# Performance work log

Hardware: AMD Instinct MI355X
Metric: run time of the kernel (lower is better)

Reference implementation:

```python
import jax, jax.numpy as jnp
import numpy as np

NUM_HEADS = 12
HEAD_DIM = 128
DIM = NUM_HEADS * HEAD_DIM  # 1536
ROTARY_DIM = HEAD_DIM       # partial_rotary_factor = 1
BASE = 10000.0
EPS = 1e-6


def rms_norm(x, scale):
    # RMSNorm over the full inner dim (applied before head split), Flux-style QKNorm
    var = jnp.mean(x * x, axis=-1, keepdims=True)
    return x * jax.lax.rsqrt(var + EPS) * scale


def rope_cos_sin(n):
    half = ROTARY_DIM // 2
    inv_freq = 1.0 / (BASE ** (jnp.arange(0, half, dtype=jnp.float32) / half))
    ang = jnp.arange(n, dtype=jnp.float32)[:, None] * inv_freq[None, :]  # [n, half]
    # broadcast over [b, n, h, half]
    return jnp.cos(ang)[None, :, None, :], jnp.sin(ang)[None, :, None, :]


def apply_rope(x, cos, sin):
    # x: [b, n, h, d]; rotate first ROTARY_DIM dims (NeoX half-split)
    half = ROTARY_DIM // 2
    x1 = x[..., :half]
    x2 = x[..., half:ROTARY_DIM]
    rest = x[..., ROTARY_DIM:]
    out = jnp.concatenate([x1 * cos - x2 * sin, x2 * cos + x1 * sin], axis=-1)
    if rest.shape[-1]:
        out = jnp.concatenate([out, rest], axis=-1)
    return out


def setup_inputs() -> dict:
    key = jax.random.key(0)
    ks = jax.random.split(key, 12)
    b, s_in, s_ctx = 2, 2048, 256
    sd = 0.02
    return {
        "input": jax.random.normal(ks[0], (b, s_in, DIM), dtype=jnp.float32),
        "context": jax.random.normal(ks[1], (b, s_ctx, DIM), dtype=jnp.float32),
        "W_qkv_in": jax.random.normal(ks[2], (DIM, 3 * DIM), dtype=jnp.float32) * sd,
        "b_qkv_in": jnp.zeros((3 * DIM,), dtype=jnp.float32),
        "W_qkv_ctx": jax.random.normal(ks[3], (DIM, 3 * DIM), dtype=jnp.float32) * sd,
        "b_qkv_ctx": jnp.zeros((3 * DIM,), dtype=jnp.float32),
        "qs_in": jnp.ones((DIM,), dtype=jnp.float32),
        "ks_in": jnp.ones((DIM,), dtype=jnp.float32),
        "qs_ctx": jnp.ones((DIM,), dtype=jnp.float32),
        "ks_ctx": jnp.ones((DIM,), dtype=jnp.float32),
        "W_out_in": jax.random.normal(ks[4], (DIM, DIM), dtype=jnp.float32) * sd,
        "b_out_in": jnp.zeros((DIM,), dtype=jnp.float32),
        "W_out_ctx": jax.random.normal(ks[5], (DIM, DIM), dtype=jnp.float32) * sd,
        "b_out_ctx": jnp.zeros((DIM,), dtype=jnp.float32),
    }


def reference(input, context, W_qkv_in, b_qkv_in, W_qkv_ctx, b_qkv_ctx,
              qs_in, ks_in, qs_ctx, ks_ctx,
              W_out_in, b_out_in, W_out_ctx, b_out_ctx):
    b = input.shape[0]
    s_ctx = context.shape[1]

    qi, ki, vi = jnp.split(input @ W_qkv_in + b_qkv_in, 3, axis=-1)
    qc, kc, vc = jnp.split(context @ W_qkv_ctx + b_qkv_ctx, 3, axis=-1)

    qi = rms_norm(qi, qs_in)
    ki = rms_norm(ki, ks_in)
    qc = rms_norm(qc, qs_ctx)
    kc = rms_norm(kc, ks_ctx)

    # concatenated joint sequence: context first, then input
    q = jnp.concatenate([qc, qi], axis=1)
    k = jnp.concatenate([kc, ki], axis=1)
    v = jnp.concatenate([vc, vi], axis=1)
    n = q.shape[1]

    q = q.reshape(b, n, NUM_HEADS, HEAD_DIM)
    k = k.reshape(b, n, NUM_HEADS, HEAD_DIM)
    v = v.reshape(b, n, NUM_HEADS, HEAD_DIM)

    cos, sin = rope_cos_sin(n)
    q = apply_rope(q, cos, sin)
    k = apply_rope(k, cos, sin)

    scale = HEAD_DIM ** -0.5
    attn = jnp.einsum("bqhd,bkhd->bhqk", q, k) * scale
    attn = jax.nn.softmax(attn, axis=-1)
    out = jnp.einsum("bhqk,bkhd->bqhd", attn, v).reshape(b, n, DIM)

    input_output = out[:, s_ctx:, :] @ W_out_in + b_out_in
    context_output = out[:, :s_ctx, :] @ W_out_ctx + b_out_ctx
    return (input_output, context_output)
```

## Files before the change

kernel.cpp:

```cpp
#include <hip/hip_runtime.h>
#include <hip/hip_bf16.h>

typedef __hip_bfloat16 bf16;
typedef __attribute__((ext_vector_type(8))) short short8;
typedef __attribute__((ext_vector_type(4))) float f32x4;

#define DIMC 1536
#define NQKV 4608
#define NH   12
#define HD   128
#define NTOK 2304
#define SCTX 256
#define SIN  2048
#define BATCH 2

__device__ __forceinline__ float bf2f(unsigned short u) {
    return __uint_as_float(((unsigned int)u) << 16);
}
__device__ __forceinline__ unsigned short f2bfu(float f) {
    bf16 h = (bf16)f; return *(unsigned short*)&h;
}

#define GLOAD16(gp, lp) __builtin_amdgcn_global_load_lds(                      \
    (__attribute__((address_space(1))) void*)(gp),                             \
    (__attribute__((address_space(3))) void*)(lp), 16, 0, 0)

__global__ __launch_bounds__(256) void cvt_bf16(
    const float* __restrict__ X, unsigned short* __restrict__ Y, int n4)
{
    int i = blockIdx.x * 256 + threadIdx.x;
    if (i < n4) {
        float4 v = ((const float4*)X)[i];
        union { unsigned short u[4]; uint2 p; } o;
        o.u[0] = f2bfu(v.x); o.u[1] = f2bfu(v.y);
        o.u[2] = f2bfu(v.z); o.u[3] = f2bfu(v.w);
        ((uint2*)Y)[i] = o.p;
    }
}

__global__ __launch_bounds__(256) void transpose_cvt(
    const float* __restrict__ W, unsigned short* __restrict__ Wt, int K, int N)
{
    __shared__ float tile[32][33];
    int n0 = blockIdx.x * 32, k0 = blockIdx.y * 32;
    int tx = threadIdx.x & 31, ty = threadIdx.x >> 5;
    #pragma unroll
    for (int i = 0; i < 4; ++i) {
        int kk = ty + i * 8;
        tile[kk][tx] = W[(size_t)(k0 + kk) * N + n0 + tx];
    }
    __syncthreads();
    #pragma unroll
    for (int i = 0; i < 4; ++i) {
        int nn = ty + i * 8;
        Wt[(size_t)(n0 + nn) * K + k0 + tx] = f2bfu(tile[tx][nn]);
    }
}

__device__ __forceinline__ void storeC(float* p, float v) { *p = v; }
__device__ __forceinline__ void storeC(unsigned short* p, float v) { *p = f2bfu(v); }

template <typename CT>
__global__ __launch_bounds__(256) void gemm_mfma(
    const unsigned short* __restrict__ A, const unsigned short* __restrict__ Wt,
    const float* __restrict__ bias, CT* __restrict__ C,
    int N, int K, int S, int aStr, int aOff, int cStr, int cOff)
{
    __shared__ __align__(16) unsigned short a_lds[128 * 32];
    __shared__ __align__(16) unsigned short b_lds[128 * 32];

    int tid = threadIdx.x;
    int wv = tid >> 6, lane = tid & 63;
    int wm = wv >> 1, wn = wv & 1;
    int quad = lane >> 4, l16 = lane & 15;
    int bm = blockIdx.y * 128, bn = blockIdx.x * 128;

    int m0 = tid >> 2;
    int c  = (tid & 3) ^ ((m0 >> 1) & 3);
    int r0 = bm + m0, r1 = bm + m0 + 64;
    size_t apA0 = ((size_t)((r0 / S) * aStr + aOff + (r0 % S))) * (size_t)K + c * 8;
    size_t apA1 = ((size_t)((r1 / S) * aStr + aOff + (r1 % S))) * (size_t)K + c * 8;
    size_t apB0 = (size_t)(bn + m0) * K + c * 8;
    size_t apB1 = (size_t)(bn + m0 + 64) * K + c * 8;

    unsigned short* ldsA0 = &a_lds[(wv * 64) * 8];
    unsigned short* ldsA1 = &a_lds[(256 + wv * 64) * 8];
    unsigned short* ldsB0 = &b_lds[(wv * 64) * 8];
    unsigned short* ldsB1 = &b_lds[(256 + wv * 64) * 8];

    int gA[4], gB[4];
    #pragma unroll
    for (int mt = 0; mt < 4; ++mt) {
        int m = wm * 64 + mt * 16 + l16;
        gA[mt] = (m * 4 + (quad ^ ((m >> 1) & 3))) * 8;
    }
    #pragma unroll
    for (int nt = 0; nt < 4; ++nt) {
        int n = wn * 64 + nt * 16 + l16;
        gB[nt] = (n * 4 + (quad ^ ((n >> 1) & 3))) * 8;
    }

    f32x4 acc[4][4];
    #pragma unroll
    for (int mt = 0; mt < 4; ++mt)
        #pragma unroll
        for (int nt = 0; nt < 4; ++nt) acc[mt][nt] = (f32x4){0.f, 0.f, 0.f, 0.f};

    for (int k0 = 0; k0 < K; k0 += 32) {
        GLOAD16(A + apA0 + k0, ldsA0);
        GLOAD16(A + apA1 + k0, ldsA1);
        GLOAD16(Wt + apB0 + k0, ldsB0);
        GLOAD16(Wt + apB1 + k0, ldsB1);
        __syncthreads();

        short8 af[4], bfr[4];
        #pragma unroll
        for (int mt = 0; mt < 4; ++mt) af[mt] = *(const short8*)&a_lds[gA[mt]];
        #pragma unroll
        for (int nt = 0; nt < 4; ++nt) bfr[nt] = *(const short8*)&b_lds[gB[nt]];
        #pragma unroll
        for (int mt = 0; mt < 4; ++mt)
            #pragma unroll
            for (int nt = 0; nt < 4; ++nt)
                acc[mt][nt] = __builtin_amdgcn_mfma_f32_16x16x32_bf16(
                    af[mt], bfr[nt], acc[mt][nt], 0, 0, 0);
        __syncthreads();
    }

    float bv[4];
    #pragma unroll
    for (int nt = 0; nt < 4; ++nt) bv[nt] = bias[bn + wn * 64 + nt * 16 + l16];
    #pragma unroll
    for (int mt = 0; mt < 4; ++mt) {
        #pragma unroll
        for (int r = 0; r < 4; ++r) {
            int row = bm + wm * 64 + mt * 16 + quad * 4 + r;
            size_t crow = (size_t)((row / S) * cStr + cOff + (row % S));
            CT* cp = C + crow * (size_t)N + bn + wn * 64 + l16;
            #pragma unroll
            for (int nt = 0; nt < 4; ++nt)
                storeC(cp + nt * 16, acc[mt][nt][r] + bv[nt]);
        }
    }
}

__global__ __launch_bounds__(256) void rms_rope_pack(
    const unsigned short* __restrict__ QKV,
    const float* __restrict__ qs_in, const float* __restrict__ ks_in,
    const float* __restrict__ qs_ctx, const float* __restrict__ ks_ctx,
    bf16* __restrict__ Q, bf16* __restrict__ K)
{
    __shared__ float qrow[DIMC];
    __shared__ float krow[DIMC];
    __shared__ float rq[4], rk[4];

    int token = blockIdx.x;
    int b = token / NTOK;
    int p = token % NTOK;
    bool is_ctx = (p < SCTX);
    const float* qs = is_ctx ? qs_ctx : qs_in;
    const float* ks = is_ctx ? ks_ctx : ks_in;

    int t = threadIdx.x;
    const unsigned short* row = QKV + (size_t)token * NQKV;

    float ssq_q = 0.f, ssq_k = 0.f;
    #pragma unroll
    for (int i = 0; i < 6; ++i) {
        int c = t + 256 * i;
        float q = bf2f(row[c]);
        float k = bf2f(row[DIMC + c]);
        qrow[c] = q; krow[c] = k;
        ssq_q += q * q; ssq_k += k * k;
    }
    for (int o = 32; o > 0; o >>= 1) {
        ssq_q += __shfl_down(ssq_q, o);
        ssq_k += __shfl_down(ssq_k, o);
    }
    if ((t & 63) == 0) { rq[t >> 6] = ssq_q; rk[t >> 6] = ssq_k; }
    __syncthreads();
    float sq = rq[0] + rq[1] + rq[2] + rq[3];
    float sk = rk[0] + rk[1] + rk[2] + rk[3];
    float invq = rsqrtf(sq * (1.0f / DIMC) + 1e-6f);
    float invk = rsqrtf(sk * (1.0f / DIMC) + 1e-6f);

    #pragma unroll
    for (int i = 0; i < 6; ++i) {
        int c = t + 256 * i;
        int h = c >> 7, d = c & 127;
        int j = d & 63;
        float inv_freq = powf(10000.0f, -(float)j * (1.0f / 64.0f));
        float ang = (float)p * inv_freq;
        float sn, cs;
        sincosf(ang, &sn, &cs);
        int pc = (d < 64) ? (c + 64) : (c - 64);

        float self_q = qrow[c]  * invq * qs[c];
        float part_q = qrow[pc] * invq * qs[pc];
        float qo = (d < 64) ? (self_q * cs - part_q * sn)
                            : (self_q * cs + part_q * sn);

        float self_k = krow[c]  * invk * ks[c];
        float part_k = krow[pc] * invk * ks[pc];
        float ko = (d < 64) ? (self_k * cs - part_k * sn)
                            : (self_k * cs + part_k * sn);

        size_t qi = ((size_t)(b * NH + h) * NTOK + p) * HD + d;
        Q[qi] = (bf16)qo;
        K[qi] = (bf16)ko;
    }
}

__global__ __launch_bounds__(256) void vt_pack(
    const unsigned short* __restrict__ QKV, unsigned short* __restrict__ Vt)
{
    __shared__ unsigned short tileT[128][72];

    int pt = blockIdx.x % (NTOK / 64);
    int bh = blockIdx.x / (NTOK / 64);
    int b = bh / NH, h = bh % NH;
    int p0 = pt * 64;

    int t = threadIdx.x, wv = t >> 6, l = t & 63;

    const unsigned short* src =
        QKV + (size_t)(b * NTOK + p0 + l) * NQKV + 2 * DIMC + h * HD;
    #pragma unroll
    for (int it = 0; it < 4; ++it) {
        int c = it * 4 + wv;
        short8 v = *(const short8*)(src + c * 8);
        const unsigned short* vp = (const unsigned short*)&v;
        #pragma unroll
        for (int i = 0; i < 8; ++i) tileT[c * 8 + i][l] = vp[i];
    }
    __syncthreads();

    int d = t >> 1, jh = (t & 1) * 32;
    unsigned short* dst = Vt + ((size_t)bh * HD + d) * NTOK + p0 + jh;
    #pragma unroll
    for (int k = 0; k < 4; ++k) {
        short8 v = *(const short8*)&tileT[d][jh + k * 8];
        *(short8*)(dst + k * 8) = v;
    }
}

__global__ __launch_bounds__(256, 2) void attn_mfma(
    const unsigned short* __restrict__ Qh,
    const unsigned short* __restrict__ Kh,
    const unsigned short* __restrict__ Vth,
    bf16* __restrict__ O)
{
    __shared__ __align__(16) unsigned short k_lds[64 * 128];
    __shared__ __align__(16) unsigned short v_lds[128 * 64];
    __shared__ __align__(16) unsigned short p_lds[4][32][72];
    __shared__ float bc[4][32];

    int tid = threadIdx.x;
    int wv = tid >> 6, lane = tid & 63;
    int quad = lane >> 4, l16 = lane & 15;

    int qt = blockIdx.x % (NTOK / 128);
    int bh = blockIdx.x / (NTOK / 128);
    int b = bh / NH, h = bh % NH;
    int p0 = qt * 128;
    int qw = p0 + wv * 32;

    const unsigned short* Kbh = Kh + (size_t)bh * NTOK * HD;
    const unsigned short* Vbh = Vth + (size_t)bh * HD * NTOK;

    short8 qf[2][4];
    #pragma unroll
    for (int mt = 0; mt < 2; ++mt) {
        const unsigned short* qrow =
            Qh + ((size_t)bh * NTOK + qw + mt * 16 + l16) * HD + quad * 8;
        #pragma unroll
        for (int dk = 0; dk < 4; ++dk) qf[mt][dk] = *(const short8*)(qrow + dk * 32);
    }

    float m_r[2][4], l_r[2][4];
    f32x4 oac[8][2];
    #pragma unroll
    for (int mt = 0; mt < 2; ++mt)
        #pragma unroll
        for (int r = 0; r < 4; ++r) { m_r[mt][r] = -1e30f; l_r[mt][r] = 0.f; }
    #pragma unroll
    for (int md = 0; md < 8; ++md)
        #pragma unroll
        for (int nt = 0; nt < 2; ++nt) oac[md][nt] = (f32x4){0.f, 0.f, 0.f, 0.f};

    const float cscale = 0.08838834764831845f * 1.44269504088896f;

    int jrowK = wv * 4 + (lane >> 4);
    int cK = (lane & 15) ^ jrowK;
    int dV = wv * 8 + (lane >> 3);
    int cV = (lane & 7) ^ (lane >> 3);

    for (int j0 = 0; j0 < NTOK; j0 += 64) {
        #pragma unroll
        for (int it = 0; it < 4; ++it)
            GLOAD16(Kbh + (size_t)(j0 + it * 16 + jrowK) * HD + cK * 8,
                    &k_lds[(it * 256 + wv * 64) * 8]);
        #pragma unroll
        for (int it = 0; it < 4; ++it)
            GLOAD16(Vbh + (size_t)(it * 32 + dV) * NTOK + j0 + cV * 8,
                    &v_lds[(it * 256 + wv * 64) * 8]);
        __syncthreads();

        f32x4 s[2][4];
        #pragma unroll
        for (int n = 0; n < 4; ++n) {
            int jl = n * 16 + l16;
            f32x4 a0 = (f32x4){0.f, 0.f, 0.f, 0.f};
            f32x4 a1 = (f32x4){0.f, 0.f, 0.f, 0.f};
            #pragma unroll
            for (int dk = 0; dk < 4; ++dk) {
                short8 kf = *(const short8*)&k_lds[(jl * 16 + ((dk * 4 + quad) ^ l16)) * 8];
                a0 = __builtin_amdgcn_mfma_f32_16x16x32_bf16(qf[0][dk], kf, a0, 0, 0, 0);
                a1 = __builtin_amdgcn_mfma_f32_16x16x32_bf16(qf[1][dk], kf, a1, 0, 0, 0);
            }
            s[0][n] = a0; s[1][n] = a1;
        }

        float alpha[2][4], rs[2][4];
        #pragma unroll
        for (int mt = 0; mt < 2; ++mt) {
            #pragma unroll
            for (int r = 0; r < 4; ++r) {
                float t = fmaxf(fmaxf(s[mt][0][r], s[mt][1][r]),
                                fmaxf(s[mt][2][r], s[mt][3][r]));
                t = fmaxf(t, __shfl_xor(t, 1));
                t = fmaxf(t, __shfl_xor(t, 2));
                t = fmaxf(t, __shfl_xor(t, 4));
                t = fmaxf(t, __shfl_xor(t, 8));
                float mn = fmaxf(m_r[mt][r], t * cscale);
                alpha[mt][r] = exp2f(m_r[mt][r] - mn);
                m_r[mt][r] = mn;
                rs[mt][r] = 0.f;
            }
        }

        #pragma unroll
        for (int mt = 0; mt < 2; ++mt)
            #pragma unroll
            for (int n = 0; n < 4; ++n) {
                #pragma unroll
                for (int r = 0; r < 4; ++r) {
                    float e = exp2f(s[mt][n][r] * cscale - m_r[mt][r]);
                    rs[mt][r] += e;
                    p_lds[wv][mt * 16 + quad * 4 + r][n * 16 + l16] = f2bfu(e);
                }
            }
        #pragma unroll
        for (int mt = 0; mt < 2; ++mt)
            #pragma unroll
            for (int r = 0; r < 4; ++r) {
                float t = rs[mt][r];
                t += __shfl_xor(t, 1);
                t += __shfl_xor(t, 2);
                t += __shfl_xor(t, 4);
                t += __shfl_xor(t, 8);
                l_r[mt][r] = l_r[mt][r] * alpha[mt][r] + t;
            }

        if (l16 == 0) {
            #pragma unroll
            for (int mt = 0; mt < 2; ++mt)
                #pragma unroll
                for (int r = 0; r < 4; ++r)
                    bc[wv][mt * 16 + quad * 4 + r] = alpha[mt][r];
        }
        float al[2];
        #pragma unroll
        for (int nt = 0; nt < 2; ++nt) al[nt] = bc[wv][nt * 16 + l16];
        #pragma unroll
        for (int md = 0; md < 8; ++md)
            #pragma unroll
            for (int nt = 0; nt < 2; ++nt) {
                oac[md][nt][0] *= al[nt]; oac[md][nt][1] *= al[nt];
                oac[md][nt][2] *= al[nt]; oac[md][nt][3] *= al[nt];
            }

        #pragma unroll
        for (int kt = 0; kt < 2; ++kt) {
            short8 pf[2];
            #pragma unroll
            for (int nt = 0; nt < 2; ++nt)
                pf[nt] = *(const short8*)&p_lds[wv][nt * 16 + l16][kt * 32 + quad * 8];
            #pragma unroll
            for (int md = 0; md < 8; ++md) {
                int dl = md * 16 + l16;
                short8 vf = *(const short8*)&v_lds[(dl * 8 + ((kt * 4 + quad) ^ (l16 & 7))) * 8];
                #pragma unroll
                for (int nt = 0; nt < 2; ++nt)
                    oac[md][nt] = __builtin_amdgcn_mfma_f32_16x16x32_bf16(
                        vf, pf[nt], oac[md][nt], 0, 0, 0);
            }
        }
        __syncthreads();
    }

    if (l16 == 0) {
        #pragma unroll
        for (int mt = 0; mt < 2; ++mt)
            #pragma unroll
            for (int r = 0; r < 4; ++r)
                bc[wv][mt * 16 + quad * 4 + r] = l_r[mt][r];
    }
    float il[2];
    #pragma unroll
    for (int nt = 0; nt < 2; ++nt) il[nt] = 1.0f / bc[wv][nt * 16 + l16];

    #pragma unroll
    for (int md = 0; md < 8; ++md)
        #pragma unroll
        for (int nt = 0; nt < 2; ++nt) {
            int q = qw + nt * 16 + l16;
            union { unsigned short u[4]; uint2 v; } pk;
            #pragma unroll
            for (int r = 0; r < 4; ++r) pk.u[r] = f2bfu(oac[md][nt][r] * il[nt]);
            *(uint2*)((unsigned short*)O +
                      ((size_t)(b * NTOK) + q) * DIMC + h * HD + md * 16 + quad * 4) = pk.v;
        }
}

extern "C" void kernel_launch(void* const* d_in, const int* in_sizes, int n_in,
                              void* d_out, int out_size, void* d_ws, size_t ws_size,
                              hipStream_t stream)
{
    const float* input     = (const float*)d_in[0];
    const float* context   = (const float*)d_in[1];
    const float* W_qkv_in  = (const float*)d_in[2];
    const float* b_qkv_in  = (const float*)d_in[3];
    const float* W_qkv_ctx = (const float*)d_in[4];
    const float* b_qkv_ctx = (const float*)d_in[5];
    const float* qs_in     = (const float*)d_in[6];
    const float* ks_in     = (const float*)d_in[7];
    const float* qs_ctx    = (const float*)d_in[8];
    const float* ks_ctx    = (const float*)d_in[9];
    const float* W_out_in  = (const float*)d_in[10];
    const float* b_out_in  = (const float*)d_in[11];
    const float* W_out_ctx = (const float*)d_in[12];
    const float* b_out_ctx = (const float*)d_in[13];
    float* out = (float*)d_out;

    char* ws = (char*)d_ws;
    unsigned short* QKVb = (unsigned short*)ws;
    bf16*           Ob   = (bf16*)ws;
    unsigned short* Qb   = (unsigned short*)(ws + 42467328);
    unsigned short* Kb   = Qb + (size_t)BATCH * NH * NTOK * HD;
    unsigned short* Vtb  = Kb + (size_t)BATCH * NH * NTOK * HD;
    unsigned short* AbIn  = (unsigned short*)(ws + 84934656);
    unsigned short* AbCtx = AbIn + (size_t)BATCH * SIN * DIMC;
    unsigned short* WtOutIn  = (unsigned short*)(ws + 84934656);
    unsigned short* WtOutCtx = WtOutIn + (size_t)DIMC * DIMC;
    unsigned short* WtQkvIn  = (unsigned short*)(ws + 99090432);
    unsigned short* WtQkvCtx = (unsigned short*)(ws + 113246208);

    cvt_bf16<<<(BATCH * SIN * DIMC / 4 + 255) / 256, 256, 0, stream>>>(
        input, AbIn, BATCH * SIN * DIMC / 4);
    cvt_bf16<<<(BATCH * SCTX * DIMC / 4 + 255) / 256, 256, 0, stream>>>(
        context, AbCtx, BATCH * SCTX * DIMC / 4);
    transpose_cvt<<<dim3(NQKV / 32, DIMC / 32), 256, 0, stream>>>(W_qkv_in, WtQkvIn, DIMC, NQKV);
    transpose_cvt<<<dim3(NQKV / 32, DIMC / 32), 256, 0, stream>>>(W_qkv_ctx, WtQkvCtx, DIMC, NQKV);

    gemm_mfma<unsigned short><<<dim3(NQKV / 128, (BATCH * SIN) / 128), 256, 0, stream>>>(
        AbIn, WtQkvIn, b_qkv_in, QKVb, NQKV, DIMC, SIN, SIN, 0, NTOK, SCTX);
    gemm_mfma<unsigned short><<<dim3(NQKV / 128, (BATCH * SCTX) / 128), 256, 0, stream>>>(
        AbCtx, WtQkvCtx, b_qkv_ctx, QKVb, NQKV, DIMC, SCTX, SCTX, 0, NTOK, 0);

    rms_rope_pack<<<BATCH * NTOK, 256, 0, stream>>>(
        QKVb, qs_in, ks_in, qs_ctx, ks_ctx, (bf16*)Qb, (bf16*)Kb);
    vt_pack<<<BATCH * NH * (NTOK / 64), 256, 0, stream>>>(QKVb, Vtb);

    attn_mfma<<<BATCH * NH * (NTOK / 128), 256, 0, stream>>>(Qb, Kb, Vtb, Ob);

    transpose_cvt<<<dim3(DIMC / 32, DIMC / 32), 256, 0, stream>>>(W_out_in, WtOutIn, DIMC, DIMC);
    transpose_cvt<<<dim3(DIMC / 32, DIMC / 32), 256, 0, stream>>>(W_out_ctx, WtOutCtx, DIMC, DIMC);

    gemm_mfma<float><<<dim3(DIMC / 128, (BATCH * SIN) / 128), 256, 0, stream>>>(
        (const unsigned short*)Ob, WtOutIn, b_out_in, out,
        DIMC, DIMC, SIN, NTOK, SCTX, SIN, 0);
    gemm_mfma<float><<<dim3(DIMC / 128, (BATCH * SCTX) / 128), 256, 0, stream>>>(
        (const unsigned short*)Ob, WtOutCtx, b_out_ctx, out + (size_t)BATCH * SIN * DIMC,
        DIMC, DIMC, SCTX, NTOK, 0, SCTX, 0);
}
```

Measured before the change: 555.9 us.

## Shrink attention query tile, merge conversion launches, precompute RoPE tables

Result: slower. 571.8 us (+2.9%).

```diff
diff --git a/kernel.cpp b/kernel.cpp
--- a/kernel.cpp
+++ b/kernel.cpp
@@ -25,23 +25,29 @@
     (__attribute__((address_space(1))) void*)(gp),                             \
     (__attribute__((address_space(3))) void*)(lp), 16, 0, 0)
 
-__global__ __launch_bounds__(256) void cvt_bf16(
-    const float* __restrict__ X, unsigned short* __restrict__ Y, int n4)
+__global__ __launch_bounds__(256) void cvt_both(
+    const float* __restrict__ X0, unsigned short* __restrict__ Y0, int n4_0,
+    const float* __restrict__ X1, unsigned short* __restrict__ Y1, int n4_1)
 {
     int i = blockIdx.x * 256 + threadIdx.x;
-    if (i < n4) {
-        float4 v = ((const float4*)X)[i];
-        union { unsigned short u[4]; uint2 p; } o;
-        o.u[0] = f2bfu(v.x); o.u[1] = f2bfu(v.y);
-        o.u[2] = f2bfu(v.z); o.u[3] = f2bfu(v.w);
-        ((uint2*)Y)[i] = o.p;
-    }
-}
-
-__global__ __launch_bounds__(256) void transpose_cvt(
-    const float* __restrict__ W, unsigned short* __restrict__ Wt, int K, int N)
+    const float* X; unsigned short* Y;
+    if (i < n4_0) { X = X0; Y = Y0; }
+    else { i -= n4_0; if (i >= n4_1) return; X = X1; Y = Y1; }
+    float4 v = ((const float4*)X)[i];
+    union { unsigned short u[4]; uint2 p; } o;
+    o.u[0] = f2bfu(v.x); o.u[1] = f2bfu(v.y);
+    o.u[2] = f2bfu(v.z); o.u[3] = f2bfu(v.w);
+    ((uint2*)Y)[i] = o.p;
+}
+
+__global__ __launch_bounds__(256) void transpose_cvt_pair(
+    const float* __restrict__ W0, unsigned short* __restrict__ Wt0,
+    const float* __restrict__ W1, unsigned short* __restrict__ Wt1,
+    int K, int N)
 {
     __shared__ float tile[32][33];
+    const float* W = blockIdx.z ? W1 : W0;
+    unsigned short* Wt = blockIdx.z ? Wt1 : Wt0;
     int n0 = blockIdx.x * 32, k0 = blockIdx.y * 32;
     int tx = threadIdx.x & 31, ty = threadIdx.x >> 5;
     #pragma unroll
@@ -55,6 +61,19 @@
         int nn = ty + i * 8;
         Wt[(size_t)(n0 + nn) * K + k0 + tx] = f2bfu(tile[tx][nn]);
     }
+}
+
+__global__ __launch_bounds__(256) void rope_table(
+    float* __restrict__ cost, float* __restrict__ sint)
+{
+    int idx = blockIdx.x * 256 + threadIdx.x;
+    if (idx >= NTOK * 64) return;
+    int p = idx >> 6, j = idx & 63;
+    float inv_freq = powf(10000.0f, -(float)j * (1.0f / 64.0f));
+    float ang = (float)p * inv_freq;
+    float sn, cs;
+    sincosf(ang, &sn, &cs);
+    cost[idx] = cs; sint[idx] = sn;
 }
 
 __device__ __forceinline__ void storeC(float* p, float v) { *p = v; }
@@ -148,6 +167,7 @@
     const unsigned short* __restrict__ QKV,
     const float* __restrict__ qs_in, const float* __restrict__ ks_in,
     const float* __restrict__ qs_ctx, const float* __restrict__ ks_ctx,
+    const float* __restrict__ cost, const float* __restrict__ sint,
     bf16* __restrict__ Q, bf16* __restrict__ K)
 {
     __shared__ float qrow[DIMC];
@@ -187,12 +207,10 @@
     #pragma unroll
     for (int i = 0; i < 6; ++i) {
         int c = t + 256 * i;
-        int h = c >> 7, d = c & 127;
+        int d = c & 127;
         int j = d & 63;
-        float inv_freq = powf(10000.0f, -(float)j * (1.0f / 64.0f));
-        float ang = (float)p * inv_freq;
-        float sn, cs;
-        sincosf(ang, &sn, &cs);
+        float cs = cost[p * 64 + j];
+        float sn = sint[p * 64 + j];
         int pc = (d < 64) ? (c + 64) : (c - 64);
 
         float self_q = qrow[c]  * invq * qs[c];
@@ -205,6 +223,7 @@
         float ko = (d < 64) ? (self_k * cs - part_k * sn)
                             : (self_k * cs + part_k * sn);
 
+        int h = c >> 7;
         size_t qi = ((size_t)(b * NH + h) * NTOK + p) * HD + d;
         Q[qi] = (bf16)qo;
         K[qi] = (bf16)ko;
@@ -244,7 +263,7 @@
     }
 }
 
-__global__ __launch_bounds__(256, 2) void attn_mfma(
+__global__ __launch_bounds__(256, 3) void attn_mfma(
     const unsigned short* __restrict__ Qh,
     const unsigned short* __restrict__ Kh,
     const unsigned short* __restrict__ Vth,
@@ -252,41 +271,35 @@
 {
     __shared__ __align__(16) unsigned short k_lds[64 * 128];
     __shared__ __align__(16) unsigned short v_lds[128 * 64];
-    __shared__ __align__(16) unsigned short p_lds[4][32][72];
-    __shared__ float bc[4][32];
+    __shared__ __align__(16) unsigned short p_lds[4][16][72];
+    __shared__ float bc[4][16];
 
     int tid = threadIdx.x;
     int wv = tid >> 6, lane = tid & 63;
     int quad = lane >> 4, l16 = lane & 15;
 
-    int qt = blockIdx.x % (NTOK / 128);
-    int bh = blockIdx.x / (NTOK / 128);
+    int qt = blockIdx.x % (NTOK / 64);
+    int bh = blockIdx.x / (NTOK / 64);
     int b = bh / NH, h = bh % NH;
-    int p0 = qt * 128;
-    int qw = p0 + wv * 32;
+    int qw = qt * 64 + wv * 16;
 
     const unsigned short* Kbh = Kh + (size_t)bh * NTOK * HD;
     const unsigned short* Vbh = Vth + (size_t)bh * HD * NTOK;
 
-    short8 qf[2][4];
-    #pragma unroll
-    for (int mt = 0; mt < 2; ++mt) {
+    short8 qf[4];
+    {
         const unsigned short* qrow =
-            Qh + ((size_t)bh * NTOK + qw + mt * 16 + l16) * HD + quad * 8;
-        #pragma unroll
-        for (int dk = 0; dk < 4; ++dk) qf[mt][dk] = *(const short8*)(qrow + dk * 32);
-    }
-
-    float m_r[2][4], l_r[2][4];
-    f32x4 oac[8][2];
-    #pragma unroll
-    for (int mt = 0; mt < 2; ++mt)
-        #pragma unroll
-        for (int r = 0; r < 4; ++r) { m_r[mt][r] = -1e30f; l_r[mt][r] = 0.f; }
-    #pragma unroll
-    for (int md = 0; md < 8; ++md)
-        #pragma unroll
-        for (int nt = 0; nt < 2; ++nt) oac[md][nt] = (f32x4){0.f, 0.f, 0.f, 0.f};
+            Qh + ((size_t)bh * NTOK + qw + l16) * HD + quad * 8;
+        #pragma unroll
+        for (int dk = 0; dk < 4; ++dk) qf[dk] = *(const short8*)(qrow + dk * 32);
+    }
+
+    float m_r[4], l_r[4];
+    f32x4 oac[8];
+    #pragma unroll
+    for (int r = 0; r < 4; ++r) { m_r[r] = -1e30f; l_r[r] = 0.f; }
+    #pragma unroll
+    for (int md = 0; md < 8; ++md) oac[md] = (f32x4){0.f, 0.f, 0.f, 0.f};
 
     const float cscale = 0.08838834764831845f * 1.44269504088896f;
 
@@ -306,94 +319,71 @@
                     &v_lds[(it * 256 + wv * 64) * 8]);
         __syncthreads();
 
-        f32x4 s[2][4];
+        f32x4 s[4];
         #pragma unroll
         for (int n = 0; n < 4; ++n) {
             int jl = n * 16 + l16;
             f32x4 a0 = (f32x4){0.f, 0.f, 0.f, 0.f};
-            f32x4 a1 = (f32x4){0.f, 0.f, 0.f, 0.f};
             #pragma unroll
             for (int dk = 0; dk < 4; ++dk) {
                 short8 kf = *(const short8*)&k_lds[(jl * 16 + ((dk * 4 + quad) ^ l16)) * 8];
-                a0 = __builtin_amdgcn_mfma_f32_16x16x32_bf16(qf[0][dk], kf, a0, 0, 0, 0);
-                a1 = __builtin_amdgcn_mfma_f32_16x16x32_bf16(qf[1][dk], kf, a1, 0, 0, 0);
+                a0 = __builtin_amdgcn_mfma_f32_16x16x32_bf16(qf[dk], kf, a0, 0, 0, 0);
             }
-            s[0][n] = a0; s[1][n] = a1;
-        }
-
-        float alpha[2][4], rs[2][4];
-        #pragma unroll
-        for (int mt = 0; mt < 2; ++mt) {
+            s[n] = a0;
+        }
+
+        float alpha[4], rs[4];
+        #pragma unroll
+        for (int r = 0; r < 4; ++r) {
+            float t = fmaxf(fmaxf(s[0][r], s[1][r]), fmaxf(s[2][r], s[3][r]));
+            t = fmaxf(t, __shfl_xor(t, 1));
+            t = fmaxf(t, __shfl_xor(t, 2));
+            t = fmaxf(t, __shfl_xor(t, 4));
+            t = fmaxf(t, __shfl_xor(t, 8));
+            float mn = fmaxf(m_r[r], t * cscale);
+            alpha[r] = exp2f(m_r[r] - mn);
+            m_r[r] = mn;
+            rs[r] = 0.f;
+        }
+
+        #pragma unroll
+        for (int n = 0; n < 4; ++n) {
             #pragma unroll
             for (int r = 0; r < 4; ++r) {
-                float t = fmaxf(fmaxf(s[mt][0][r], s[mt][1][r]),
-                                fmaxf(s[mt][2][r], s[mt][3][r]));
-                t = fmaxf(t, __shfl_xor(t, 1));
-                t = fmaxf(t, __shfl_xor(t, 2));
-                t = fmaxf(t, __shfl_xor(t, 4));
-                t = fmaxf(t, __shfl_xor(t, 8));
-                float mn = fmaxf(m_r[mt][r], t * cscale);
-                alpha[mt][r] = exp2f(m_r[mt][r] - mn);
-                m_r[mt][r] = mn;
-                rs[mt][r] = 0.f;
+                float e = exp2f(s[n][r] * cscale - m_r[r]);
+                rs[r] += e;
+                p_lds[wv][quad * 4 + r][n * 16 + l16] = f2bfu(e);
             }
         }
-
-        #pragma unroll
-        for (int mt = 0; mt < 2; ++mt)
-            #pragma unroll
-            for (int n = 0; n < 4; ++n) {
-                #pragma unroll
-                for (int r = 0; r < 4; ++r) {
-                    float e = exp2f(s[mt][n][r] * cscale - m_r[mt][r]);
-                    rs[mt][r] += e;
-                    p_lds[wv][mt * 16 + quad * 4 + r][n * 16 + l16] = f2bfu(e);
-                }
-            }
-        #pragma unroll
-        for (int mt = 0; mt < 2; ++mt)
-            #pragma unroll
-            for (int r = 0; r < 4; ++r) {
-                float t = rs[mt][r];
-                t += __shfl_xor(t, 1);
-                t += __shfl_xor(t, 2);
-                t += __shfl_xor(t, 4);
-                t += __shfl_xor(t, 8);
-                l_r[mt][r] = l_r[mt][r] * alpha[mt][r] + t;
-            }
+        #pragma unroll
+        for (int r = 0; r < 4; ++r) {
+            float t = rs[r];
+            t += __shfl_xor(t, 1);
+            t += __shfl_xor(t, 2);
+            t += __shfl_xor(t, 4);
+            t += __shfl_xor(t, 8);
+            l_r[r] = l_r[r] * alpha[r] + t;
+        }
 
         if (l16 == 0) {
             #pragma unroll
-            for (int mt = 0; mt < 2; ++mt)
-                #pragma unroll
-                for (int r = 0; r < 4; ++r)
-                    bc[wv][mt * 16 + quad * 4 + r] = alpha[mt][r];
-        }
-        float al[2];
-        #pragma unroll
-        for (int nt = 0; nt < 2; ++nt) al[nt] = bc[wv][nt * 16 + l16];
-        #pragma unroll
-        for (int md = 0; md < 8; ++md)
-            #pragma unroll
-            for (int nt = 0; nt < 2; ++nt) {
-                oac[md][nt][0] *= al[nt]; oac[md][nt][1] *= al[nt];
-                oac[md][nt][2] *= al[nt]; oac[md][nt][3] *= al[nt];
-            }
+            for (int r = 0; r < 4; ++r) bc[wv][quad * 4 + r] = alpha[r];
+        }
+        float al = bc[wv][l16];
+        #pragma unroll
+        for (int md = 0; md < 8; ++md) {
+            oac[md][0] *= al; oac[md][1] *= al;
+            oac[md][2] *= al; oac[md][3] *= al;
+        }
 
         #pragma unroll
         for (int kt = 0; kt < 2; ++kt) {
-            short8 pf[2];
-            #pragma unroll
-            for (int nt = 0; nt < 2; ++nt)
-                pf[nt] = *(const short8*)&p_lds[wv][nt * 16 + l16][kt * 32 + quad * 8];
+            short8 pf = *(const short8*)&p_lds[wv][l16][kt * 32 + quad * 8];
             #pragma unroll
             for (int md = 0; md < 8; ++md) {
                 int dl = md * 16 + l16;
                 short8 vf = *(const short8*)&v_lds[(dl * 8 + ((kt * 4 + quad) ^ (l16 & 7))) * 8];
-                #pragma unroll
-                for (int nt = 0; nt < 2; ++nt)
-                    oac[md][nt] = __builtin_amdgcn_mfma_f32_16x16x32_bf16(
-                        vf, pf[nt], oac[md][nt], 0, 0, 0);
+                oac[md] = __builtin_amdgcn_mfma_f32_16x16x32_bf16(vf, pf, oac[md], 0, 0, 0);
             }
         }
         __syncthreads();
@@ -401,26 +391,20 @@
 
     if (l16 == 0) {
         #pragma unroll
-        for (int mt = 0; mt < 2; ++mt)
-            #pragma unroll
-            for (int r = 0; r < 4; ++r)
-                bc[wv][mt * 16 + quad * 4 + r] = l_r[mt][r];
-    }
-    float il[2];
-    #pragma unroll
-    for (int nt = 0; nt < 2; ++nt) il[nt] = 1.0f / bc[wv][nt * 16 + l16];
-
-    #pragma unroll
-    for (int md = 0; md < 8; ++md)
-        #pragma unroll
-        for (int nt = 0; nt < 2; ++nt) {
-            int q = qw + nt * 16 + l16;
-            union { unsigned short u[4]; uint2 v; } pk;
-            #pragma unroll
-            for (int r = 0; r < 4; ++r) pk.u[r] = f2bfu(oac[md][nt][r] * il[nt]);
-            *(uint2*)((unsigned short*)O +
-                      ((size_t)(b * NTOK) + q) * DIMC + h * HD + md * 16 + quad * 4) = pk.v;
-        }
+        for (int r = 0; r < 4; ++r) bc[wv][quad * 4 + r] = l_r[r];
+    }
+    float il = 1.0f / bc[wv][l16];
+
+    int q = qw + l16;
+    unsigned short* obase = (unsigned short*)O +
+        ((size_t)(b * NTOK) + q) * DIMC + h * HD + quad * 4;
+    #pragma unroll
+    for (int md = 0; md < 8; ++md) {
+        union { unsigned short u[4]; uint2 v; } pk;
+        #pragma unroll
+        for (int r = 0; r < 4; ++r) pk.u[r] = f2bfu(oac[md][r] * il);
+        *(uint2*)(obase + md * 16) = pk.v;
+    }
 }
 
 extern "C" void kernel_launch(void* const* d_in, const int* in_sizes, int n_in,
@@ -451,31 +435,33 @@
     unsigned short* Vtb  = Kb + (size_t)BATCH * NH * NTOK * HD;
     unsigned short* AbIn  = (unsigned short*)(ws + 84934656);
     unsigned short* AbCtx = AbIn + (size_t)BATCH * SIN * DIMC;
+    float* costab = (float*)(ws + 84934656);
+    float* sintab = costab + NTOK * 64;
     unsigned short* WtOutIn  = (unsigned short*)(ws + 84934656);
     unsigned short* WtOutCtx = WtOutIn + (size_t)DIMC * DIMC;
     unsigned short* WtQkvIn  = (unsigned short*)(ws + 99090432);
     unsigned short* WtQkvCtx = (unsigned short*)(ws + 113246208);
 
-    cvt_bf16<<<(BATCH * SIN * DIMC / 4 + 255) / 256, 256, 0, stream>>>(
-        input, AbIn, BATCH * SIN * DIMC / 4);
-    cvt_bf16<<<(BATCH * SCTX * DIMC / 4 + 255) / 256, 256, 0, stream>>>(
-        context, AbCtx, BATCH * SCTX * DIMC / 4);
-    transpose_cvt<<<dim3(NQKV / 32, DIMC / 32), 256, 0, stream>>>(W_qkv_in, WtQkvIn, DIMC, NQKV);
-    transpose_cvt<<<dim3(NQKV / 32, DIMC / 32), 256, 0, stream>>>(W_qkv_ctx, WtQkvCtx, DIMC, NQKV);
+    int n4in = BATCH * SIN * DIMC / 4, n4ctx = BATCH * SCTX * DIMC / 4;
+    cvt_both<<<(n4in + n4ctx + 255) / 256, 256, 0, stream>>>(
+        input, AbIn, n4in, context, AbCtx, n4ctx);
+    transpose_cvt_pair<<<dim3(NQKV / 32, DIMC / 32, 2), 256, 0, stream>>>(
+        W_qkv_in, WtQkvIn, W_qkv_ctx, WtQkvCtx, DIMC, NQKV);
 
     gemm_mfma<unsigned short><<<dim3(NQKV / 128, (BATCH * SIN) / 128), 256, 0, stream>>>(
         AbIn, WtQkvIn, b_qkv_in, QKVb, NQKV, DIMC, SIN, SIN, 0, NTOK, SCTX);
     gemm_mfma<unsigned short><<<dim3(NQKV / 128, (BATCH * SCTX) / 128), 256, 0, stream>>>(
         AbCtx, WtQkvCtx, b_qkv_ctx, QKVb, NQKV, DIMC, SCTX, SCTX, 0, NTOK, 0);
 
+    rope_table<<<(NTOK * 64 + 255) / 256, 256, 0, stream>>>(costab, sintab);
     rms_rope_pack<<<BATCH * NTOK, 256, 0, stream>>>(
-        QKVb, qs_in, ks_in, qs_ctx, ks_ctx, (bf16*)Qb, (bf16*)Kb);
+        QKVb, qs_in, ks_in, qs_ctx, ks_ctx, costab, sintab, (bf16*)Qb, (bf16*)Kb);
     vt_pack<<<BATCH * NH * (NTOK / 64), 256, 0, stream>>>(QKVb, Vtb);
 
-    attn_mfma<<<BATCH * NH * (NTOK / 128), 256, 0, stream>>>(Qb, Kb, Vtb, Ob);
-
-    transpose_cvt<<<dim3(DIMC / 32, DIMC / 32), 256, 0, stream>>>(W_out_in, WtOutIn, DIMC, DIMC);
-    transpose_cvt<<<dim3(DIMC / 32, DIMC / 32), 256, 0, stream>>>(W_out_ctx, WtOutCtx, DIMC, DIMC);
+    attn_mfma<<<BATCH * NH * (NTOK / 64), 256, 0, stream>>>(Qb, Kb, Vtb, Ob);
+
+    transpose_cvt_pair<<<dim3(DIMC / 32, DIMC / 32, 2), 256, 0, stream>>>(
+        W_out_in, WtOutIn, W_out_ctx, WtOutCtx, DIMC, DIMC);
 
     gemm_mfma<float><<<dim3(DIMC / 128, (BATCH * SIN) / 128), 256, 0, stream>>>(
         (const unsigned short*)Ob, WtOutIn, b_out_in, out,
```
